# Optimization experiments

Hardware: AMD Instinct MI355X
Metric: run time of the kernel (lower is better)

The kernel has to match this reference:

```python
import jax, jax.numpy as jnp
import numpy as np

EPS_INTERP = 1e-8
EPS_BN = 1e-5


def _bn_relu(x, gamma, beta):
    # x: [B, C, N]; training-mode BatchNorm1d over (B, N) with biased variance
    mean = jnp.mean(x, axis=(0, 2), keepdims=True)
    var = jnp.mean((x - mean) ** 2, axis=(0, 2), keepdims=True)
    xn = (x - mean) / jnp.sqrt(var + EPS_BN)
    return jax.nn.relu(xn * gamma[None, :, None] + beta[None, :, None])


def setup_inputs() -> dict:
    key = jax.random.key(0)
    ks = jax.random.split(key, 8)
    B, N, S, D = 16, 4096, 1024, 128
    return {
        "xyz1": jax.random.normal(ks[0], (B, 3, N), jnp.float32),
        "xyz2": jax.random.normal(ks[1], (B, 3, S), jnp.float32),
        "points1": jax.random.normal(ks[2], (B, D, N), jnp.float32),
        "points2": jax.random.normal(ks[3], (B, D, S), jnp.float32),
        "w0": jax.random.normal(ks[4], (256, 512), jnp.float32) * 0.04,
        "b0": jax.random.normal(ks[5], (256,), jnp.float32) * 0.01,
        "gamma0": jnp.ones((256,), jnp.float32),
        "beta0": jnp.zeros((256,), jnp.float32),
        "w1": jax.random.normal(ks[6], (128, 256), jnp.float32) * 0.06,
        "b1": jax.random.normal(ks[7], (128,), jnp.float32) * 0.01,
        "gamma1": jnp.ones((128,), jnp.float32),
        "beta1": jnp.zeros((128,), jnp.float32),
    }


def reference(xyz1, xyz2, points1, points2, w0, b0, gamma0, beta0, w1, b1, gamma1, beta1):
    # to [B, N, C] layouts
    x1 = jnp.transpose(xyz1, (0, 2, 1))   # [B, N, 3]
    x2 = jnp.transpose(xyz2, (0, 2, 1))   # [B, S, 3]
    p2 = jnp.transpose(points2, (0, 2, 1))  # [B, S, D]
    B, N, _ = x1.shape

    # squared pairwise distances [B, N, S]
    dists = (jnp.sum(x1 ** 2, -1)[:, :, None]
             + jnp.sum(x2 ** 2, -1)[:, None, :]
             - 2.0 * jnp.einsum('bnc,bsc->bns', x1, x2))

    # 3 nearest neighbors (ascending distance)
    neg_d, idx = jax.lax.top_k(-dists, 3)   # idx: [B, N, 3]
    d3 = -neg_d
    recip = 1.0 / (d3 + EPS_INTERP)
    weight = recip / jnp.sum(recip, axis=2, keepdims=True)  # [B, N, 3]

    # gather neighbor features: [B, N, 3, D]
    gathered = jax.vmap(lambda p, i: p[i])(p2, idx)
    # NOTE: this repo flattens the 3 weighted neighbors (no sum) -> [B, N, 3*D]
    interp = (gathered * weight[..., None]).reshape(B, N, -1)

    new_pts = jnp.concatenate([jnp.transpose(points1, (0, 2, 1)), interp], axis=-1)  # [B, N, 512]
    x = jnp.transpose(new_pts, (0, 2, 1))  # [B, 512, N]

    x = _bn_relu(jnp.einsum('oc,bcn->bon', w0, x) + b0[None, :, None], gamma0, beta0)
    x = _bn_relu(jnp.einsum('oc,bcn->bon', w1, x) + b1[None, :, None], gamma1, beta1)
    return x
```

## Files before the change

kernel.cpp:

```cpp
#include <hip/hip_runtime.h>
#include <stdint.h>

typedef unsigned short ushort_t;
typedef __attribute__((ext_vector_type(8))) __bf16 bf16x8;
typedef __attribute__((ext_vector_type(4))) float f32x4;

__device__ __forceinline__ float b2f(ushort_t u) {
    unsigned v = ((unsigned)u) << 16;
    float f;
    __builtin_memcpy(&f, &v, 4);
    return f;
}

__device__ __forceinline__ ushort_t f2b(float f) {
    __bf16 h = (__bf16)f;
    return __builtin_bit_cast(ushort_t, h);
}

__device__ __forceinline__ void gl_lds16(const void* g, void* l) {
    __builtin_amdgcn_global_load_lds((const __attribute__((address_space(1))) void*)g,
                                     (__attribute__((address_space(3))) void*)l, 16, 0, 0);
}

__global__ __launch_bounds__(256) void k_pre(const float* __restrict__ w0, ushort_t* __restrict__ w0b,
                                             const float* __restrict__ w1, ushort_t* __restrict__ w1b,
                                             const float* __restrict__ xyz2, float4* __restrict__ sdat,
                                             const float* __restrict__ points2, ushort_t* __restrict__ p2t) {
    int bid = blockIdx.x;
    int t = threadIdx.x;
    if (bid < 512) {
        int i = bid * 256 + t;
        w0b[i] = f2b(w0[i]);
    } else if (bid < 640) {
        int i = (bid - 512) * 256 + t;
        w1b[i] = f2b(w1[i]);
    } else if (bid < 704) {
        int bb = bid - 640;
        int b = bb & 15, by = bb >> 4;
        int s = by * 256 + t;
        const float* x2 = xyz2 + (size_t)b * 3 * 1024;
        float x = x2[s], y = x2[1024 + s], z = x2[2048 + s];
        float4 v;
        v.x = x; v.y = y; v.z = z;
        v.w = __fadd_rn(__fadd_rn(__fmul_rn(x, x), __fmul_rn(y, y)), __fmul_rn(z, z));
        sdat[(size_t)b * 1024 + s] = v;
    } else {
        int bb = bid - 704;
        int b = bb & 15, sy = bb >> 4;
        int s = sy * 64 + (t & 63);
        int g = t >> 6;
        const float* src = points2 + (size_t)b * 128 * 1024 + s;
        ushort_t* dst = p2t + ((size_t)b * 1024 + s) * 128;
#pragma unroll
        for (int i = 0; i < 4; ++i) {
            int cp = i * 4 + g;
            ushort_t tmp[8];
#pragma unroll
            for (int k = 0; k < 8; ++k) tmp[k] = f2b(src[(size_t)(cp * 8 + k) * 1024]);
            *(uint4*)(dst + cp * 8) = *(const uint4*)tmp;
        }
    }
}

__global__ __launch_bounds__(256) void k_interp(const float* __restrict__ xyz1,
                                                const float4* __restrict__ sdat,
                                                const float* __restrict__ points1,
                                                const ushort_t* __restrict__ p2t,
                                                ushort_t* __restrict__ X) {
    int b = blockIdx.x;
    int n0 = blockIdx.y * 32;
    int t = threadIdx.x;
    int tq = t & 31;
    int slice = t >> 5;
    int wave = t >> 6, lane = t & 63;

    __shared__ __align__(16) char sbuf[16384];
    float4* sP = (float4*)sbuf;
    int*   sidx = (int*)sbuf;
    float* sw   = (float*)(sbuf + 384);
    __shared__ float sD[256 * 3];
    __shared__ int   sI[256 * 3];

    {
        const float4* src = sdat + (size_t)b * 1024;
#pragma unroll
        for (int c = 0; c < 4; ++c) {
            int p = wave * 256 + c * 64 + lane;
            gl_lds16(src + p, sbuf + p * 16);
        }
    }

    int n = n0 + tq;
    float x = xyz1[((size_t)b * 3 + 0) * 4096 + n];
    float y = xyz1[((size_t)b * 3 + 1) * 4096 + n];
    float z = xyz1[((size_t)b * 3 + 2) * 4096 + n];
    float s1 = __fadd_rn(__fadd_rn(__fmul_rn(x, x), __fmul_rn(y, y)), __fmul_rn(z, z));

    __syncthreads();

    const float* p1base = points1 + (size_t)b * 128 * 4096 + n0 + tq;
    float p1v[16];
#pragma unroll
    for (int i = 0; i < 2; ++i)
#pragma unroll
        for (int k = 0; k < 8; ++k)
            p1v[i * 8 + k] = p1base[(size_t)(((i * 8 + slice) * 8) + k) * 4096];

    float d0 = 1e30f, d1 = 1e30f, d2 = 1e30f;
    int i0 = 0, i1 = 0, i2 = 0;
    int sbeg = slice * 128;
    const float4* sdL = sP + sbeg;
#pragma unroll 8
    for (int s = 0; s < 128; ++s) {
        float4 v = sdL[s];
        float dot = fmaf(z, v.z, fmaf(y, v.y, __fmul_rn(x, v.x)));
        float d = __fadd_rn(fmaf(-2.0f, dot, s1), v.w);
        int si = sbeg + s;
        bool c0 = d < d0, c1 = d < d1, c2 = d < d2;
        i2 = c1 ? i1 : (c2 ? si : i2);
        i1 = c0 ? i0 : (c1 ? si : i1);
        i0 = c0 ? si : i0;
        d2 = fminf(fmaxf(d, d1), d2);
        d1 = fminf(fmaxf(d, d0), d1);
        d0 = fminf(d, d0);
    }
    sD[t * 3 + 0] = d0; sD[t * 3 + 1] = d1; sD[t * 3 + 2] = d2;
    sI[t * 3 + 0] = i0; sI[t * 3 + 1] = i1; sI[t * 3 + 2] = i2;

    {
        ushort_t* dstbase = X + (size_t)(b * 4096 + n0 + tq) * 512;
#pragma unroll
        for (int i = 0; i < 2; ++i) {
            int piece = i * 8 + slice;
            ushort_t tmp[8];
#pragma unroll
            for (int k = 0; k < 8; ++k) tmp[k] = f2b(p1v[i * 8 + k]);
            *(uint4*)(dstbase + piece * 8) = *(const uint4*)tmp;
        }
    }
    __syncthreads();

    if (t < 32) {
        int sel0 = -1, sel1 = -1;
        float seld[3]; int seli[3];
#pragma unroll
        for (int r = 0; r < 3; ++r) {
            float bd = 1e38f; int bi = 1 << 30;
            for (int k = 0; k < 24; ++k) {
                int s3 = (k * 0xAAAB) >> 17;
                int rank = k - s3 * 3;
                int base = (s3 * 32 + t) * 3 + rank;
                float cd = sD[base];
                int ci = sI[base];
                bool excl = (ci == sel0) | (ci == sel1);
                bool better = (!excl) & ((cd < bd) | ((cd == bd) & (ci < bi)));
                if (better) { bd = cd; bi = ci; }
            }
            seld[r] = bd; seli[r] = bi;
            if (r == 0) sel0 = bi; else if (r == 1) sel1 = bi;
        }
        float r0 = 1.0f / (seld[0] + 1e-8f);
        float r1 = 1.0f / (seld[1] + 1e-8f);
        float r2 = 1.0f / (seld[2] + 1e-8f);
        float rs = r0 + r1 + r2;
        sw[t * 3 + 0] = r0 / rs; sw[t * 3 + 1] = r1 / rs; sw[t * 3 + 2] = r2 / rs;
        sidx[t * 3 + 0] = seli[0]; sidx[t * 3 + 1] = seli[1]; sidx[t * 3 + 2] = seli[2];
    }
    __syncthreads();

#pragma unroll
    for (int i = 0; i < 6; ++i) {
        int idx = i * 256 + t;
        int q = idx / 48;
        int rem = idx - q * 48;
        int r = rem >> 4;
        int piece = rem & 15;
        int si = sidx[q * 3 + r];
        float wt = sw[q * 3 + r];
        const ushort_t* src = p2t + ((size_t)b * 1024 + si) * 128 + piece * 8;
        uint4 raw = *(const uint4*)src;
        ushort_t* e = (ushort_t*)&raw;
        ushort_t outv[8];
#pragma unroll
        for (int k = 0; k < 8; ++k) outv[k] = f2b(wt * b2f(e[k]));
        ushort_t* dst = X + (size_t)(b * 4096 + n0 + q) * 512 + 128 + r * 128 + piece * 8;
        *(uint4*)dst = *(const uint4*)outv;
    }
}

__global__ __launch_bounds__(256) void k_gemm(const ushort_t* __restrict__ A,
                                              const ushort_t* __restrict__ Bt,
                                              const float* __restrict__ bias,
                                              ushort_t* __restrict__ Y,
                                              float* __restrict__ part_s,
                                              float* __restrict__ part_q,
                                              int Mtot, int K) {
    __shared__ __align__(16) char smem[35840];
    ushort_t* As = (ushort_t*)smem;
    ushort_t* Bs = (ushort_t*)(smem + 16384);
    ushort_t* sY = (ushort_t*)smem;
    float* red_s = (float*)(smem + 34816);
    float* red_q = red_s + 128;

    int t = threadIdx.x;
    int m0 = blockIdx.x * 128;
    int j0 = blockIdx.y * 128;
    int wave = t >> 6, lane = t & 63;
    int wm = wave >> 1, wn = wave & 1;
    int l16 = lane & 15, quad = lane >> 4;

    if (t < 128) { red_s[t] = 0.f; red_q[t] = 0.f; }

    f32x4 acc[4][4] = {};

    int nk = K >> 6;
    for (int kt = 0; kt < nk; ++kt) {
#pragma unroll
        for (int c = 0; c < 4; ++c) {
            int idx = c * 256 + t;
            int row = idx >> 3, kc = idx & 7;
            gl_lds16(A + (size_t)(m0 + row) * K + kt * 64 + kc * 8, As + idx * 8);
            gl_lds16(Bt + (size_t)(j0 + row) * K + kt * 64 + kc * 8, Bs + idx * 8);
        }
        __syncthreads();

#pragma unroll
        for (int kk = 0; kk < 2; ++kk) {
            bf16x8 af[4], bfr[4];
#pragma unroll
            for (int mi = 0; mi < 4; ++mi)
                af[mi] = *(const bf16x8*)(As + (wm * 64 + mi * 16 + l16) * 64 + kk * 32 + quad * 8);
#pragma unroll
            for (int ni = 0; ni < 4; ++ni)
                bfr[ni] = *(const bf16x8*)(Bs + (wn * 64 + ni * 16 + l16) * 64 + kk * 32 + quad * 8);
#pragma unroll
            for (int mi = 0; mi < 4; ++mi)
#pragma unroll
                for (int ni = 0; ni < 4; ++ni)
                    acc[mi][ni] = __builtin_amdgcn_mfma_f32_16x16x32_bf16(af[mi], bfr[ni], acc[mi][ni], 0, 0, 0);
        }
        __syncthreads();
    }

#pragma unroll
    for (int mi = 0; mi < 4; ++mi) {
        int obase = wm * 64 + mi * 16 + quad * 4;
        float bv[4];
#pragma unroll
        for (int r = 0; r < 4; ++r) bv[r] = bias[m0 + obase + r];
        float sr[4] = {0.f, 0.f, 0.f, 0.f}, qr[4] = {0.f, 0.f, 0.f, 0.f};
#pragma unroll
        for (int ni = 0; ni < 4; ++ni) {
            int j_local = wn * 64 + ni * 16 + l16;
            ushort4 pk;
            float v0 = acc[mi][ni][0] + bv[0];
            float v1 = acc[mi][ni][1] + bv[1];
            float v2 = acc[mi][ni][2] + bv[2];
            float v3 = acc[mi][ni][3] + bv[3];
            pk.x = f2b(v0); pk.y = f2b(v1); pk.z = f2b(v2); pk.w = f2b(v3);
            sr[0] += v0; qr[0] += v0 * v0;
            sr[1] += v1; qr[1] += v1 * v1;
            sr[2] += v2; qr[2] += v2 * v2;
            sr[3] += v3; qr[3] += v3 * v3;
            *(ushort4*)(sY + j_local * 136 + obase) = pk;
        }
#pragma unroll
        for (int r = 0; r < 4; ++r) {
            float s = sr[r], q = qr[r];
            s += __shfl_xor(s, 1); s += __shfl_xor(s, 2);
            s += __shfl_xor(s, 4); s += __shfl_xor(s, 8);
            q += __shfl_xor(q, 1); q += __shfl_xor(q, 2);
            q += __shfl_xor(q, 4); q += __shfl_xor(q, 8);
            if (l16 == 0) {
                atomicAdd(&red_s[obase + r], s);
                atomicAdd(&red_q[obase + r], q);
            }
        }
    }
    __syncthreads();

#pragma unroll
    for (int rep = 0; rep < 8; ++rep) {
        int idx = rep * 256 + t;
        int jl = idx >> 4;
        int o8 = idx & 15;
        uint4 vv = *(const uint4*)(sY + jl * 136 + o8 * 8);
        *(uint4*)(Y + (size_t)(j0 + jl) * Mtot + m0 + o8 * 8) = vv;
    }
    if (t < 128) {
        part_s[(size_t)blockIdx.y * Mtot + m0 + t] = red_s[t];
        part_q[(size_t)blockIdx.y * Mtot + m0 + t] = red_q[t];
    }
}

__global__ __launch_bounds__(256) void k_gemmf(const ushort_t* __restrict__ A,
                                               const ushort_t* __restrict__ Y0,
                                               const float* __restrict__ bias,
                                               const float* __restrict__ act_a,
                                               const float* __restrict__ act_b,
                                               ushort_t* __restrict__ Y,
                                               float* __restrict__ part_s,
                                               float* __restrict__ part_q,
                                               int Mtot, int K) {
    __shared__ __align__(16) char smem[35840];
    ushort_t* As = (ushort_t*)smem;
    ushort_t* Bs = (ushort_t*)(smem + 16384);
    float* sa = (float*)(smem + 32768);
    float* sb = (float*)(smem + 33792);
    ushort_t* sY = (ushort_t*)smem;
    float* red_s = (float*)(smem + 34816);
    float* red_q = red_s + 128;

    int t = threadIdx.x;
    int m0 = blockIdx.x * 128;
    int j0 = blockIdx.y * 128;
    int wave = t >> 6, lane = t & 63;
    int wm = wave >> 1, wn = wave & 1;
    int l16 = lane & 15, quad = lane >> 4;

    sa[t] = act_a[t]; sb[t] = act_b[t];
    if (t < 128) { red_s[t] = 0.f; red_q[t] = 0.f; }
    __syncthreads();

    f32x4 acc[4][4] = {};

    int nk = K >> 6;
    for (int kt = 0; kt < nk; ++kt) {
#pragma unroll
        for (int c = 0; c < 4; ++c) {
            int idx = c * 256 + t;
            int row = idx >> 3, kc = idx & 7;
            gl_lds16(A + (size_t)(m0 + row) * K + kt * 64 + kc * 8, As + idx * 8);
        }
#pragma unroll
        for (int c = 0; c < 4; ++c) {
            int idx = c * 256 + t;
            int row = idx >> 3, kc = idx & 7;
            int cbase = kt * 64 + kc * 8;
            uint4 raw = *(const uint4*)(Y0 + (size_t)(j0 + row) * K + cbase);
            ushort_t* e = (ushort_t*)&raw;
            ushort_t outv[8];
#pragma unroll
            for (int k = 0; k < 8; ++k) {
                float v = fmaxf(sa[cbase + k] * b2f(e[k]) + sb[cbase + k], 0.f);
                outv[k] = f2b(v);
            }
            *(uint4*)(Bs + idx * 8) = *(const uint4*)outv;
        }
        __syncthreads();

#pragma unroll
        for (int kk = 0; kk < 2; ++kk) {
            bf16x8 af[4], bfr[4];
#pragma unroll
            for (int mi = 0; mi < 4; ++mi)
                af[mi] = *(const bf16x8*)(As + (wm * 64 + mi * 16 + l16) * 64 + kk * 32 + quad * 8);
#pragma unroll
            for (int ni = 0; ni < 4; ++ni)
                bfr[ni] = *(const bf16x8*)(Bs + (wn * 64 + ni * 16 + l16) * 64 + kk * 32 + quad * 8);
#pragma unroll
            for (int mi = 0; mi < 4; ++mi)
#pragma unroll
                for (int ni = 0; ni < 4; ++ni)
                    acc[mi][ni] = __builtin_amdgcn_mfma_f32_16x16x32_bf16(af[mi], bfr[ni], acc[mi][ni], 0, 0, 0);
        }
        __syncthreads();
    }

#pragma unroll
    for (int mi = 0; mi < 4; ++mi) {
        int obase = wm * 64 + mi * 16 + quad * 4;
        float bv[4];
#pragma unroll
        for (int r = 0; r < 4; ++r) bv[r] = bias[m0 + obase + r];
        float sr[4] = {0.f, 0.f, 0.f, 0.f}, qr[4] = {0.f, 0.f, 0.f, 0.f};
#pragma unroll
        for (int ni = 0; ni < 4; ++ni) {
            int j_local = wn * 64 + ni * 16 + l16;
            ushort4 pk;
            float v0 = acc[mi][ni][0] + bv[0];
            float v1 = acc[mi][ni][1] + bv[1];
            float v2 = acc[mi][ni][2] + bv[2];
            float v3 = acc[mi][ni][3] + bv[3];
            pk.x = f2b(v0); pk.y = f2b(v1); pk.z = f2b(v2); pk.w = f2b(v3);
            sr[0] += v0; qr[0] += v0 * v0;
            sr[1] += v1; qr[1] += v1 * v1;
            sr[2] += v2; qr[2] += v2 * v2;
            sr[3] += v3; qr[3] += v3 * v3;
            *(ushort4*)(sY + j_local * 136 + obase) = pk;
        }
#pragma unroll
        for (int r = 0; r < 4; ++r) {
            float s = sr[r], q = qr[r];
            s += __shfl_xor(s, 1); s += __shfl_xor(s, 2);
            s += __shfl_xor(s, 4); s += __shfl_xor(s, 8);
            q += __shfl_xor(q, 1); q += __shfl_xor(q, 2);
            q += __shfl_xor(q, 4); q += __shfl_xor(q, 8);
            if (l16 == 0) {
                atomicAdd(&red_s[obase + r], s);
                atomicAdd(&red_q[obase + r], q);
            }
        }
    }
    __syncthreads();

#pragma unroll
    for (int rep = 0; rep < 8; ++rep) {
        int idx = rep * 256 + t;
        int jl = idx >> 4;
        int o8 = idx & 15;
        uint4 vv = *(const uint4*)(sY + jl * 136 + o8 * 8);
        *(uint4*)(Y + (size_t)(j0 + jl) * Mtot + m0 + o8 * 8) = vv;
    }
    if (t < 128) {
        part_s[(size_t)blockIdx.y * Mtot + m0 + t] = red_s[t];
        part_q[(size_t)blockIdx.y * Mtot + m0 + t] = red_q[t];
    }
}

__global__ __launch_bounds__(256) void k_bnfin(const float* __restrict__ part_s,
                                               const float* __restrict__ part_q,
                                               int nby,
                                               const float* __restrict__ gamma,
                                               const float* __restrict__ beta,
                                               float* __restrict__ a, float* __restrict__ bb,
                                               int C, float inv_count) {
    __shared__ float rs[4], rq[4];
    int i = blockIdx.x;
    int t = threadIdx.x;
    float s = 0.f, q = 0.f;
    for (int by = t; by < nby; by += 256) {
        s += part_s[(size_t)by * C + i];
        q += part_q[(size_t)by * C + i];
    }
    s += __shfl_xor(s, 1);  q += __shfl_xor(q, 1);
    s += __shfl_xor(s, 2);  q += __shfl_xor(q, 2);
    s += __shfl_xor(s, 4);  q += __shfl_xor(q, 4);
    s += __shfl_xor(s, 8);  q += __shfl_xor(q, 8);
    s += __shfl_xor(s, 16); q += __shfl_xor(q, 16);
    s += __shfl_xor(s, 32); q += __shfl_xor(q, 32);
    int wv = t >> 6, ln = t & 63;
    if (ln == 0) { rs[wv] = s; rq[wv] = q; }
    __syncthreads();
    if (t == 0) {
        s = (rs[0] + rs[1]) + (rs[2] + rs[3]);
        q = (rq[0] + rq[1]) + (rq[2] + rq[3]);
        float mean = s * inv_count;
        float var = q * inv_count - mean * mean;
        float sc = gamma[i] / sqrtf(var + 1e-5f);
        a[i] = sc;
        bb[i] = beta[i] - mean * sc;
    }
}

__global__ __launch_bounds__(256) void k_out(const ushort_t* __restrict__ Y1,
                                             const float* __restrict__ a,
                                             const float* __restrict__ bb,
                                             float* __restrict__ out) {
    __shared__ float sa[128], sb[128];
    int t = threadIdx.x;
    if (t < 128) { sa[t] = a[t]; sb[t] = bb[t]; }
    __syncthreads();
    int b = blockIdx.x;
    int nl = t & 127;
    int half = t >> 7;
    int n = blockIdx.y * 128 + nl;
    const uint4* src = (const uint4*)(Y1 + (size_t)(b * 4096 + n) * 128);
    float* dst = out + (size_t)b * 128 * 4096 + n;
    uint4 raw[8];
#pragma unroll
    for (int p = 0; p < 8; ++p) raw[p] = src[half * 8 + p];
    const ushort_t* e = (const ushort_t*)raw;
#pragma unroll
    for (int c = 0; c < 64; ++c) {
        int ch = half * 64 + c;
        float v = b2f(e[c]);
        v = fmaxf(sa[ch] * v + sb[ch], 0.f);
        dst[(size_t)ch * 4096] = v;
    }
}

extern "C" void kernel_launch(void* const* d_in, const int* in_sizes, int n_in,
                              void* d_out, int out_size, void* d_ws, size_t ws_size,
                              hipStream_t stream) {
    const float* xyz1    = (const float*)d_in[0];
    const float* xyz2    = (const float*)d_in[1];
    const float* points1 = (const float*)d_in[2];
    const float* points2 = (const float*)d_in[3];
    const float* w0      = (const float*)d_in[4];
    const float* b0      = (const float*)d_in[5];
    const float* gamma0  = (const float*)d_in[6];
    const float* beta0   = (const float*)d_in[7];
    const float* w1      = (const float*)d_in[8];
    const float* b1      = (const float*)d_in[9];
    const float* gamma1  = (const float*)d_in[10];
    const float* beta1   = (const float*)d_in[11];
    float* out = (float*)d_out;

    char* ws = (char*)d_ws;
    const size_t OFF_X    = 0;
    const size_t OFF_Y0   = 67108864;
    const size_t OFF_Y1   = 100663296;
    const size_t OFF_P2T  = 117440512;
    const size_t OFF_W0B  = 121634816;
    const size_t OFF_W1B  = 121896960;
    const size_t OFF_AB   = 121962496;
    const size_t OFF_SDAT = 121965568;
    const size_t OFF_PS0  = 122227712;
    const size_t OFF_PQ0  = 122752000;
    const size_t OFF_PS1  = 123276288;
    const size_t OFF_PQ1  = 123538432;

    ushort_t* X    = (ushort_t*)(ws + OFF_X);
    ushort_t* Y0   = (ushort_t*)(ws + OFF_Y0);
    ushort_t* Y1   = (ushort_t*)(ws + OFF_Y1);
    ushort_t* p2t  = (ushort_t*)(ws + OFF_P2T);
    ushort_t* w0b  = (ushort_t*)(ws + OFF_W0B);
    ushort_t* w1b  = (ushort_t*)(ws + OFF_W1B);
    float* ab      = (float*)(ws + OFF_AB);
    float4* sdat   = (float4*)(ws + OFF_SDAT);
    float* ps0 = (float*)(ws + OFF_PS0);
    float* pq0 = (float*)(ws + OFF_PQ0);
    float* ps1 = (float*)(ws + OFF_PS1);
    float* pq1 = (float*)(ws + OFF_PQ1);
    float* a0 = ab;       float* bb0 = ab + 256;
    float* a1 = ab + 512; float* bb1 = ab + 640;

    k_pre<<<960, 256, 0, stream>>>(w0, w0b, w1, w1b, xyz2, sdat, points2, p2t);
    k_interp<<<dim3(16, 128), 256, 0, stream>>>(xyz1, sdat, points1, p2t, X);
    k_gemm<<<dim3(2, 512), 256, 0, stream>>>(w0b, X, b0, Y0, ps0, pq0, 256, 512);
    k_bnfin<<<256, 256, 0, stream>>>(ps0, pq0, 512, gamma0, beta0, a0, bb0, 256, 1.0f / 65536.0f);
    k_gemmf<<<dim3(1, 512), 256, 0, stream>>>(w1b, Y0, b1, a0, bb0, Y1, ps1, pq1, 128, 256);
    k_bnfin<<<128, 256, 0, stream>>>(ps1, pq1, 512, gamma1, beta1, a1, bb1, 128, 1.0f / 65536.0f);
    k_out<<<dim3(16, 32), 256, 0, stream>>>(Y1, a1, bb1, out);
}
```

Baseline: 218.6 us.

## Double points per interp thread and widen first GEMM block to full output dim

k_interp now handles 64 query points per block, with each thread scanning its slice of 128 reference points for two queries, so the LDS-staged xyz2 data is loaded once per 64 points instead of per 32. The first GEMM uses 512-thread blocks covering all 256 output channels per 128-column tile. Each B (activation) tile is therefore read once instead of twice, and the epilogue is written in two halves through shared memory. The trade-off is higher register and LDS pressure, fewer blocks (1024 interp, 512 gemm) and extra barriers in the GEMM epilogue.

```diff
diff --git a/kernel.cpp b/kernel.cpp
--- a/kernel.cpp
+++ b/kernel.cpp
@@ -62,13 +62,13 @@
     }
 }
 
-__global__ __launch_bounds__(256) void k_interp(const float* __restrict__ xyz1,
-                                                const float4* __restrict__ sdat,
-                                                const float* __restrict__ points1,
-                                                const ushort_t* __restrict__ p2t,
-                                                ushort_t* __restrict__ X) {
+__global__ __launch_bounds__(256, 4) void k_interp(const float* __restrict__ xyz1,
+                                                   const float4* __restrict__ sdat,
+                                                   const float* __restrict__ points1,
+                                                   const ushort_t* __restrict__ p2t,
+                                                   ushort_t* __restrict__ X) {
     int b = blockIdx.x;
-    int n0 = blockIdx.y * 32;
+    int n0 = blockIdx.y * 64;
     int t = threadIdx.x;
     int tq = t & 31;
     int slice = t >> 5;
@@ -77,9 +77,9 @@
     __shared__ __align__(16) char sbuf[16384];
     float4* sP = (float4*)sbuf;
     int*   sidx = (int*)sbuf;
-    float* sw   = (float*)(sbuf + 384);
-    __shared__ float sD[256 * 3];
-    __shared__ int   sI[256 * 3];
+    float* sw   = (float*)(sbuf + 768);
+    __shared__ float sD[1536];
+    __shared__ int   sI[1536];
 
     {
         const float4* src = sdat + (size_t)b * 1024;
@@ -90,57 +90,90 @@
         }
     }
 
-    int n = n0 + tq;
-    float x = xyz1[((size_t)b * 3 + 0) * 4096 + n];
-    float y = xyz1[((size_t)b * 3 + 1) * 4096 + n];
-    float z = xyz1[((size_t)b * 3 + 2) * 4096 + n];
-    float s1 = __fadd_rn(__fadd_rn(__fmul_rn(x, x), __fmul_rn(y, y)), __fmul_rn(z, z));
+    int nA = n0 + tq;
+    float xA = xyz1[((size_t)b * 3 + 0) * 4096 + nA];
+    float yA = xyz1[((size_t)b * 3 + 1) * 4096 + nA];
+    float zA = xyz1[((size_t)b * 3 + 2) * 4096 + nA];
+    float s1A = __fadd_rn(__fadd_rn(__fmul_rn(xA, xA), __fmul_rn(yA, yA)), __fmul_rn(zA, zA));
+    float xB = xyz1[((size_t)b * 3 + 0) * 4096 + nA + 32];
+    float yB = xyz1[((size_t)b * 3 + 1) * 4096 + nA + 32];
+    float zB = xyz1[((size_t)b * 3 + 2) * 4096 + nA + 32];
+    float s1B = __fadd_rn(__fadd_rn(__fmul_rn(xB, xB), __fmul_rn(yB, yB)), __fmul_rn(zB, zB));
 
     __syncthreads();
 
     const float* p1base = points1 + (size_t)b * 128 * 4096 + n0 + tq;
-    float p1v[16];
+    float p1v[32];
 #pragma unroll
     for (int i = 0; i < 2; ++i)
 #pragma unroll
-        for (int k = 0; k < 8; ++k)
-            p1v[i * 8 + k] = p1base[(size_t)(((i * 8 + slice) * 8) + k) * 4096];
-
-    float d0 = 1e30f, d1 = 1e30f, d2 = 1e30f;
-    int i0 = 0, i1 = 0, i2 = 0;
+        for (int k = 0; k < 8; ++k) {
+            size_t off = (size_t)(((i * 8 + slice) * 8) + k) * 4096;
+            p1v[i * 8 + k]      = p1base[off];
+            p1v[16 + i * 8 + k] = p1base[off + 32];
+        }
+
+    float d0A = 1e30f, d1A = 1e30f, d2A = 1e30f;
+    int i0A = 0, i1A = 0, i2A = 0;
+    float d0B = 1e30f, d1B = 1e30f, d2B = 1e30f;
+    int i0B = 0, i1B = 0, i2B = 0;
     int sbeg = slice * 128;
     const float4* sdL = sP + sbeg;
-#pragma unroll 8
+#pragma unroll 4
     for (int s = 0; s < 128; ++s) {
         float4 v = sdL[s];
-        float dot = fmaf(z, v.z, fmaf(y, v.y, __fmul_rn(x, v.x)));
-        float d = __fadd_rn(fmaf(-2.0f, dot, s1), v.w);
         int si = sbeg + s;
-        bool c0 = d < d0, c1 = d < d1, c2 = d < d2;
-        i2 = c1 ? i1 : (c2 ? si : i2);
-        i1 = c0 ? i0 : (c1 ? si : i1);
-        i0 = c0 ? si : i0;
-        d2 = fminf(fmaxf(d, d1), d2);
-        d1 = fminf(fmaxf(d, d0), d1);
-        d0 = fminf(d, d0);
-    }
-    sD[t * 3 + 0] = d0; sD[t * 3 + 1] = d1; sD[t * 3 + 2] = d2;
-    sI[t * 3 + 0] = i0; sI[t * 3 + 1] = i1; sI[t * 3 + 2] = i2;
-
+        {
+            float dot = fmaf(zA, v.z, fmaf(yA, v.y, __fmul_rn(xA, v.x)));
+            float d = __fadd_rn(fmaf(-2.0f, dot, s1A), v.w);
+            bool c0 = d < d0A, c1 = d < d1A, c2 = d < d2A;
+            i2A = c1 ? i1A : (c2 ? si : i2A);
+            i1A = c0 ? i0A : (c1 ? si : i1A);
+            i0A = c0 ? si : i0A;
+            d2A = fminf(fmaxf(d, d1A), d2A);
+            d1A = fminf(fmaxf(d, d0A), d1A);
+            d0A = fminf(d, d0A);
+        }
+        {
+            float dot = fmaf(zB, v.z, fmaf(yB, v.y, __fmul_rn(xB, v.x)));
+            float d = __fadd_rn(fmaf(-2.0f, dot, s1B), v.w);
+            bool c0 = d < d0B, c1 = d < d1B, c2 = d < d2B;
+            i2B = c1 ? i1B : (c2 ? si : i2B);
+            i1B = c0 ? i0B : (c1 ? si : i1B);
+            i0B = c0 ? si : i0B;
+            d2B = fminf(fmaxf(d, d1B), d2B);
+            d1B = fminf(fmaxf(d, d0B), d1B);
+            d0B = fminf(d, d0B);
+        }
+    }
     {
-        ushort_t* dstbase = X + (size_t)(b * 4096 + n0 + tq) * 512;
+        int baseA = (slice * 64 + tq) * 3;
+        int baseB = (slice * 64 + tq + 32) * 3;
+        sD[baseA + 0] = d0A; sD[baseA + 1] = d1A; sD[baseA + 2] = d2A;
+        sI[baseA + 0] = i0A; sI[baseA + 1] = i1A; sI[baseA + 2] = i2A;
+        sD[baseB + 0] = d0B; sD[baseB + 1] = d1B; sD[baseB + 2] = d2B;
+        sI[baseB + 0] = i0B; sI[baseB + 1] = i1B; sI[baseB + 2] = i2B;
+    }
+
+    {
+        ushort_t* dstA = X + (size_t)(b * 4096 + n0 + tq) * 512;
+        ushort_t* dstB = X + (size_t)(b * 4096 + n0 + tq + 32) * 512;
 #pragma unroll
         for (int i = 0; i < 2; ++i) {
             int piece = i * 8 + slice;
-            ushort_t tmp[8];
-#pragma unroll
-            for (int k = 0; k < 8; ++k) tmp[k] = f2b(p1v[i * 8 + k]);
-            *(uint4*)(dstbase + piece * 8) = *(const uint4*)tmp;
-        }
-    }
-    __syncthreads();
-
-    if (t < 32) {
+            ushort_t tA[8], tB[8];
+#pragma unroll
+            for (int k = 0; k < 8; ++k) {
+                tA[k] = f2b(p1v[i * 8 + k]);
+                tB[k] = f2b(p1v[16 + i * 8 + k]);
+            }
+            *(uint4*)(dstA + piece * 8) = *(const uint4*)tA;
+            *(uint4*)(dstB + piece * 8) = *(const uint4*)tB;
+        }
+    }
+    __syncthreads();
+
+    if (t < 64) {
         int sel0 = -1, sel1 = -1;
         float seld[3]; int seli[3];
 #pragma unroll
@@ -149,7 +182,7 @@
             for (int k = 0; k < 24; ++k) {
                 int s3 = (k * 0xAAAB) >> 17;
                 int rank = k - s3 * 3;
-                int base = (s3 * 32 + t) * 3 + rank;
+                int base = (s3 * 64 + t) * 3 + rank;
                 float cd = sD[base];
                 int ci = sI[base];
                 bool excl = (ci == sel0) | (ci == sel1);
@@ -169,7 +202,7 @@
     __syncthreads();
 
 #pragma unroll
-    for (int i = 0; i < 6; ++i) {
+    for (int i = 0; i < 12; ++i) {
         int idx = i * 256 + t;
         int q = idx / 48;
         int rem = idx - q * 48;
@@ -188,28 +221,27 @@
     }
 }
 
-__global__ __launch_bounds__(256) void k_gemm(const ushort_t* __restrict__ A,
-                                              const ushort_t* __restrict__ Bt,
-                                              const float* __restrict__ bias,
-                                              ushort_t* __restrict__ Y,
-                                              float* __restrict__ part_s,
-                                              float* __restrict__ part_q,
-                                              int Mtot, int K) {
-    __shared__ __align__(16) char smem[35840];
+__global__ __launch_bounds__(512, 4) void k_gemm(const ushort_t* __restrict__ A,
+                                                 const ushort_t* __restrict__ Bt,
+                                                 const float* __restrict__ bias,
+                                                 ushort_t* __restrict__ Y,
+                                                 float* __restrict__ part_s,
+                                                 float* __restrict__ part_q,
+                                                 int Mtot, int K) {
+    __shared__ __align__(16) char smem[51200];
     ushort_t* As = (ushort_t*)smem;
-    ushort_t* Bs = (ushort_t*)(smem + 16384);
+    ushort_t* Bs = (ushort_t*)(smem + 32768);
     ushort_t* sY = (ushort_t*)smem;
-    float* red_s = (float*)(smem + 34816);
-    float* red_q = red_s + 128;
+    float* red_s = (float*)(smem + 49152);
+    float* red_q = red_s + 256;
 
     int t = threadIdx.x;
-    int m0 = blockIdx.x * 128;
-    int j0 = blockIdx.y * 128;
+    int j0 = blockIdx.x * 128;
     int wave = t >> 6, lane = t & 63;
     int wm = wave >> 1, wn = wave & 1;
     int l16 = lane & 15, quad = lane >> 4;
 
-    if (t < 128) { red_s[t] = 0.f; red_q[t] = 0.f; }
+    if (t < 256) { red_s[t] = 0.f; red_q[t] = 0.f; }
 
     f32x4 acc[4][4] = {};
 
@@ -217,9 +249,14 @@
     for (int kt = 0; kt < nk; ++kt) {
 #pragma unroll
         for (int c = 0; c < 4; ++c) {
-            int idx = c * 256 + t;
+            int idx = c * 512 + t;
             int row = idx >> 3, kc = idx & 7;
-            gl_lds16(A + (size_t)(m0 + row) * K + kt * 64 + kc * 8, As + idx * 8);
+            gl_lds16(A + (size_t)row * K + kt * 64 + kc * 8, As + idx * 8);
+        }
+#pragma unroll
+        for (int c = 0; c < 2; ++c) {
+            int idx = c * 512 + t;
+            int row = idx >> 3, kc = idx & 7;
             gl_lds16(Bt + (size_t)(j0 + row) * K + kt * 64 + kc * 8, Bs + idx * 8);
         }
         __syncthreads();
@@ -243,53 +280,59 @@
     }
 
 #pragma unroll
-    for (int mi = 0; mi < 4; ++mi) {
-        int obase = wm * 64 + mi * 16 + quad * 4;
-        float bv[4];
-#pragma unroll
-        for (int r = 0; r < 4; ++r) bv[r] = bias[m0 + obase + r];
-        float sr[4] = {0.f, 0.f, 0.f, 0.f}, qr[4] = {0.f, 0.f, 0.f, 0.f};
-#pragma unroll
-        for (int ni = 0; ni < 4; ++ni) {
-            int j_local = wn * 64 + ni * 16 + l16;
-            ushort4 pk;
-            float v0 = acc[mi][ni][0] + bv[0];
-            float v1 = acc[mi][ni][1] + bv[1];
-            float v2 = acc[mi][ni][2] + bv[2];
-            float v3 = acc[mi][ni][3] + bv[3];
-            pk.x = f2b(v0); pk.y = f2b(v1); pk.z = f2b(v2); pk.w = f2b(v3);
-            sr[0] += v0; qr[0] += v0 * v0;
-            sr[1] += v1; qr[1] += v1 * v1;
-            sr[2] += v2; qr[2] += v2 * v2;
-            sr[3] += v3; qr[3] += v3 * v3;
-            *(ushort4*)(sY + j_local * 136 + obase) = pk;
-        }
-#pragma unroll
-        for (int r = 0; r < 4; ++r) {
-            float s = sr[r], q = qr[r];
-            s += __shfl_xor(s, 1); s += __shfl_xor(s, 2);
-            s += __shfl_xor(s, 4); s += __shfl_xor(s, 8);
-            q += __shfl_xor(q, 1); q += __shfl_xor(q, 2);
-            q += __shfl_xor(q, 4); q += __shfl_xor(q, 8);
-            if (l16 == 0) {
-                atomicAdd(&red_s[obase + r], s);
-                atomicAdd(&red_q[obase + r], q);
+    for (int h = 0; h < 2; ++h) {
+        if ((wm >> 1) == h) {
+#pragma unroll
+            for (int mi = 0; mi < 4; ++mi) {
+                int obase = wm * 64 + mi * 16 + quad * 4;
+                int ocol = obase - h * 128;
+                float bv[4];
+#pragma unroll
+                for (int r = 0; r < 4; ++r) bv[r] = bias[obase + r];
+                float sr[4] = {0.f, 0.f, 0.f, 0.f}, qr[4] = {0.f, 0.f, 0.f, 0.f};
+#pragma unroll
+                for (int ni = 0; ni < 4; ++ni) {
+                    int j_local = wn * 64 + ni * 16 + l16;
+                    ushort4 pk;
+                    float v0 = acc[mi][ni][0] + bv[0];
+                    float v1 = acc[mi][ni][1] + bv[1];
+                    float v2 = acc[mi][ni][2] + bv[2];
+                    float v3 = acc[mi][ni][3] + bv[3];
+                    pk.x = f2b(v0); pk.y = f2b(v1); pk.z = f2b(v2); pk.w = f2b(v3);
+                    sr[0] += v0; qr[0] += v0 * v0;
+                    sr[1] += v1; qr[1] += v1 * v1;
+                    sr[2] += v2; qr[2] += v2 * v2;
+                    sr[3] += v3; qr[3] += v3 * v3;
+                    *(ushort4*)(sY + j_local * 136 + ocol) = pk;
+                }
+#pragma unroll
+                for (int r = 0; r < 4; ++r) {
+                    float s = sr[r], q = qr[r];
+                    s += __shfl_xor(s, 1); s += __shfl_xor(s, 2);
+                    s += __shfl_xor(s, 4); s += __shfl_xor(s, 8);
+                    q += __shfl_xor(q, 1); q += __shfl_xor(q, 2);
+                    q += __shfl_xor(q, 4); q += __shfl_xor(q, 8);
+                    if (l16 == 0) {
+                        atomicAdd(&red_s[obase + r], s);
+                        atomicAdd(&red_q[obase + r], q);
+                    }
+                }
             }
         }
-    }
-    __syncthreads();
-
-#pragma unroll
-    for (int rep = 0; rep < 8; ++rep) {
-        int idx = rep * 256 + t;
-        int jl = idx >> 4;
-        int o8 = idx & 15;
-        uint4 vv = *(const uint4*)(sY + jl * 136 + o8 * 8);
-        *(uint4*)(Y + (size_t)(j0 + jl) * Mtot + m0 + o8 * 8) = vv;
-    }
-    if (t < 128) {
-        part_s[(size_t)blockIdx.y * Mtot + m0 + t] = red_s[t];
-        part_q[(size_t)blockIdx.y * Mtot + m0 + t] = red_q[t];
+        __syncthreads();
+#pragma unroll
+        for (int rep = 0; rep < 4; ++rep) {
+            int idx = rep * 512 + t;
+            int jl = idx >> 4;
+            int o8 = idx & 15;
+            uint4 vv = *(const uint4*)(sY + jl * 136 + o8 * 8);
+            *(uint4*)(Y + (size_t)(j0 + jl) * Mtot + h * 128 + o8 * 8) = vv;
+        }
+        __syncthreads();
+    }
+    if (t < 256) {
+        part_s[(size_t)blockIdx.x * Mtot + t] = red_s[t];
+        part_q[(size_t)blockIdx.x * Mtot + t] = red_q[t];
     }
 }
 
@@ -527,8 +570,8 @@
     float* a1 = ab + 512; float* bb1 = ab + 640;
 
     k_pre<<<960, 256, 0, stream>>>(w0, w0b, w1, w1b, xyz2, sdat, points2, p2t);
-    k_interp<<<dim3(16, 128), 256, 0, stream>>>(xyz1, sdat, points1, p2t, X);
-    k_gemm<<<dim3(2, 512), 256, 0, stream>>>(w0b, X, b0, Y0, ps0, pq0, 256, 512);
+    k_interp<<<dim3(16, 64), 256, 0, stream>>>(xyz1, sdat, points1, p2t, X);
+    k_gemm<<<512, 512, 0, stream>>>(w0b, X, b0, Y0, ps0, pq0, 256, 512);
     k_bnfin<<<256, 256, 0, stream>>>(ps0, pq0, 512, gamma0, beta0, a0, bb0, 256, 1.0f / 65536.0f);
     k_gemmf<<<dim3(1, 512), 256, 0, stream>>>(w1b, Y0, b1, a0, bb0, Y1, ps1, pq1, 128, 256);
     k_bnfin<<<128, 256, 0, stream>>>(ps1, pq1, 512, gamma1, beta1, a1, bb1, 128, 1.0f / 65536.0f);
```

After: 212.7 us. 1.03x faster.

## Fuse neighbor gather into first GEMM and fold BN finalize via atomics

Applied to the files above, without the earlier changes.

The interpolation kernel no longer writes the 512-wide concatenated X matrix. It stores only the points1 slice plus the neighbor indices and weights, and the first GEMM gathers and weights the p2t rows while loading its B tiles. The first GEMM now uses 512-thread blocks covering all 256 output channels, and BN statistics are accumulated into global sums with atomics. This removes both k_bnfin launches, because the scale and shift are computed inside k_gemmf and k_out. The aim is to cut the large X write and read traffic and the launch overhead, at the cost of gather loads inside the GEMM loop that go through registers and are not overlapped, plus float atomics that make the sums order-nondeterministic.

```diff
diff --git a/kernel.cpp b/kernel.cpp
--- a/kernel.cpp
+++ b/kernel.cpp
@@ -25,7 +25,8 @@
 __global__ __launch_bounds__(256) void k_pre(const float* __restrict__ w0, ushort_t* __restrict__ w0b,
                                              const float* __restrict__ w1, ushort_t* __restrict__ w1b,
                                              const float* __restrict__ xyz2, float4* __restrict__ sdat,
-                                             const float* __restrict__ points2, ushort_t* __restrict__ p2t) {
+                                             const float* __restrict__ points2, ushort_t* __restrict__ p2t,
+                                             float* __restrict__ zb) {
     int bid = blockIdx.x;
     int t = threadIdx.x;
     if (bid < 512) {
@@ -44,7 +45,7 @@
         v.x = x; v.y = y; v.z = z;
         v.w = __fadd_rn(__fadd_rn(__fmul_rn(x, x), __fmul_rn(y, y)), __fmul_rn(z, z));
         sdat[(size_t)b * 1024 + s] = v;
-    } else {
+    } else if (bid < 960) {
         int bb = bid - 704;
         int b = bb & 15, sy = bb >> 4;
         int s = sy * 64 + (t & 63);
@@ -59,14 +60,18 @@
             for (int k = 0; k < 8; ++k) tmp[k] = f2b(src[(size_t)(cp * 8 + k) * 1024]);
             *(uint4*)(dst + cp * 8) = *(const uint4*)tmp;
         }
+    } else {
+        zb[t] = 0.f; zb[256 + t] = 0.f;
+        if (t < 128) { zb[512 + t] = 0.f; zb[640 + t] = 0.f; }
     }
 }
 
 __global__ __launch_bounds__(256) void k_interp(const float* __restrict__ xyz1,
                                                 const float4* __restrict__ sdat,
                                                 const float* __restrict__ points1,
-                                                const ushort_t* __restrict__ p2t,
-                                                ushort_t* __restrict__ X) {
+                                                ushort_t* __restrict__ Xp1,
+                                                int* __restrict__ sidxg,
+                                                float* __restrict__ swg) {
     int b = blockIdx.x;
     int n0 = blockIdx.y * 32;
     int t = threadIdx.x;
@@ -76,10 +81,8 @@
 
     __shared__ __align__(16) char sbuf[16384];
     float4* sP = (float4*)sbuf;
-    int*   sidx = (int*)sbuf;
-    float* sw   = (float*)(sbuf + 384);
-    __shared__ float sD[256 * 3];
-    __shared__ int   sI[256 * 3];
+    __shared__ float sD[768];
+    __shared__ int   sI[768];
 
     {
         const float4* src = sdat + (size_t)b * 1024;
@@ -128,7 +131,7 @@
     sI[t * 3 + 0] = i0; sI[t * 3 + 1] = i1; sI[t * 3 + 2] = i2;
 
     {
-        ushort_t* dstbase = X + (size_t)(b * 4096 + n0 + tq) * 512;
+        ushort_t* dstbase = Xp1 + (size_t)(b * 4096 + n0 + tq) * 128;
 #pragma unroll
         for (int i = 0; i < 2; ++i) {
             int piece = i * 8 + slice;
@@ -163,41 +166,168 @@
         float r1 = 1.0f / (seld[1] + 1e-8f);
         float r2 = 1.0f / (seld[2] + 1e-8f);
         float rs = r0 + r1 + r2;
-        sw[t * 3 + 0] = r0 / rs; sw[t * 3 + 1] = r1 / rs; sw[t * 3 + 2] = r2 / rs;
-        sidx[t * 3 + 0] = seli[0]; sidx[t * 3 + 1] = seli[1]; sidx[t * 3 + 2] = seli[2];
-    }
-    __syncthreads();
-
-#pragma unroll
-    for (int i = 0; i < 6; ++i) {
-        int idx = i * 256 + t;
-        int q = idx / 48;
-        int rem = idx - q * 48;
-        int r = rem >> 4;
-        int piece = rem & 15;
-        int si = sidx[q * 3 + r];
-        float wt = sw[q * 3 + r];
-        const ushort_t* src = p2t + ((size_t)b * 1024 + si) * 128 + piece * 8;
-        uint4 raw = *(const uint4*)src;
-        ushort_t* e = (ushort_t*)&raw;
-        ushort_t outv[8];
-#pragma unroll
-        for (int k = 0; k < 8; ++k) outv[k] = f2b(wt * b2f(e[k]));
-        ushort_t* dst = X + (size_t)(b * 4096 + n0 + q) * 512 + 128 + r * 128 + piece * 8;
-        *(uint4*)dst = *(const uint4*)outv;
-    }
-}
-
-__global__ __launch_bounds__(256) void k_gemm(const ushort_t* __restrict__ A,
-                                              const ushort_t* __restrict__ Bt,
-                                              const float* __restrict__ bias,
-                                              ushort_t* __restrict__ Y,
-                                              float* __restrict__ part_s,
-                                              float* __restrict__ part_q,
-                                              int Mtot, int K) {
+        size_t base = (size_t)(b * 4096 + n0 + t) * 3;
+        sidxg[base + 0] = seli[0]; sidxg[base + 1] = seli[1]; sidxg[base + 2] = seli[2];
+        swg[base + 0] = r0 / rs; swg[base + 1] = r1 / rs; swg[base + 2] = r2 / rs;
+    }
+}
+
+__global__ __launch_bounds__(512, 4) void k_gemm(const ushort_t* __restrict__ A,
+                                                 const ushort_t* __restrict__ Xp1,
+                                                 const ushort_t* __restrict__ p2t,
+                                                 const int* __restrict__ sidxg,
+                                                 const float* __restrict__ swg,
+                                                 const float* __restrict__ bias,
+                                                 ushort_t* __restrict__ Y,
+                                                 float* __restrict__ gs,
+                                                 float* __restrict__ gq,
+                                                 int Mtot, int K) {
+    __shared__ __align__(16) char smem[54784];
+    ushort_t* As = (ushort_t*)smem;
+    ushort_t* Bs = (ushort_t*)(smem + 32768);
+    ushort_t* sY = (ushort_t*)smem;
+    float* red_s = (float*)(smem + 49152);
+    float* red_q = red_s + 256;
+    int*   lsi   = (int*)(smem + 51200);
+    float* lsw   = (float*)(smem + 52736);
+
+    int t = threadIdx.x;
+    int j0 = blockIdx.x * 128;
+    int b = j0 >> 12;
+    int wave = t >> 6, lane = t & 63;
+    int wm = wave >> 1, wn = wave & 1;
+    int l16 = lane & 15, quad = lane >> 4;
+
+    if (t < 256) { red_s[t] = 0.f; red_q[t] = 0.f; }
+    if (t < 384) { lsi[t] = sidxg[(size_t)j0 * 3 + t]; lsw[t] = swg[(size_t)j0 * 3 + t]; }
+
+    f32x4 acc[4][4] = {};
+
+    int nk = K >> 6;
+    for (int kt = 0; kt < nk; ++kt) {
+#pragma unroll
+        for (int c = 0; c < 4; ++c) {
+            int idx = c * 512 + t;
+            int row = idx >> 3, kc = idx & 7;
+            gl_lds16(A + (size_t)row * K + kt * 64 + kc * 8, As + idx * 8);
+        }
+        if (kt < 2) {
+#pragma unroll
+            for (int c = 0; c < 2; ++c) {
+                int idx = c * 512 + t;
+                int row = idx >> 3, kc = idx & 7;
+                gl_lds16(Xp1 + (size_t)(j0 + row) * 128 + kt * 64 + kc * 8, Bs + idx * 8);
+            }
+        } else {
+            int r = (kt - 2) >> 1, h = (kt - 2) & 1;
+#pragma unroll
+            for (int c = 0; c < 2; ++c) {
+                int idx = c * 512 + t;
+                int row = idx >> 3, kc = idx & 7;
+                int si = lsi[row * 3 + r];
+                float w = lsw[row * 3 + r];
+                const ushort_t* src = p2t + ((size_t)b * 1024 + si) * 128 + h * 64 + kc * 8;
+                uint4 raw = *(const uint4*)src;
+                ushort_t* e = (ushort_t*)&raw;
+                ushort_t outv[8];
+#pragma unroll
+                for (int k = 0; k < 8; ++k) outv[k] = f2b(w * b2f(e[k]));
+                *(uint4*)(Bs + idx * 8) = *(const uint4*)outv;
+            }
+        }
+        __syncthreads();
+
+#pragma unroll
+        for (int kk = 0; kk < 2; ++kk) {
+            bf16x8 af[4], bfr[4];
+#pragma unroll
+            for (int mi = 0; mi < 4; ++mi)
+                af[mi] = *(const bf16x8*)(As + (wm * 64 + mi * 16 + l16) * 64 + kk * 32 + quad * 8);
+#pragma unroll
+            for (int ni = 0; ni < 4; ++ni)
+                bfr[ni] = *(const bf16x8*)(Bs + (wn * 64 + ni * 16 + l16) * 64 + kk * 32 + quad * 8);
+#pragma unroll
+            for (int mi = 0; mi < 4; ++mi)
+#pragma unroll
+                for (int ni = 0; ni < 4; ++ni)
+                    acc[mi][ni] = __builtin_amdgcn_mfma_f32_16x16x32_bf16(af[mi], bfr[ni], acc[mi][ni], 0, 0, 0);
+        }
+        __syncthreads();
+    }
+
+#pragma unroll
+    for (int h = 0; h < 2; ++h) {
+        if ((wm >> 1) == h) {
+#pragma unroll
+            for (int mi = 0; mi < 4; ++mi) {
+                int obase = wm * 64 + mi * 16 + quad * 4;
+                int ocol = obase - h * 128;
+                float bv[4];
+#pragma unroll
+                for (int r = 0; r < 4; ++r) bv[r] = bias[obase + r];
+                float sr[4] = {0.f, 0.f, 0.f, 0.f}, qr[4] = {0.f, 0.f, 0.f, 0.f};
+#pragma unroll
+                for (int ni = 0; ni < 4; ++ni) {
+                    int j_local = wn * 64 + ni * 16 + l16;
+                    ushort4 pk;
+                    float v0 = acc[mi][ni][0] + bv[0];
+                    float v1 = acc[mi][ni][1] + bv[1];
+                    float v2 = acc[mi][ni][2] + bv[2];
+                    float v3 = acc[mi][ni][3] + bv[3];
+                    pk.x = f2b(v0); pk.y = f2b(v1); pk.z = f2b(v2); pk.w = f2b(v3);
+                    sr[0] += v0; qr[0] += v0 * v0;
+                    sr[1] += v1; qr[1] += v1 * v1;
+                    sr[2] += v2; qr[2] += v2 * v2;
+                    sr[3] += v3; qr[3] += v3 * v3;
+                    *(ushort4*)(sY + j_local * 136 + ocol) = pk;
+                }
+#pragma unroll
+                for (int r = 0; r < 4; ++r) {
+                    float s = sr[r], q = qr[r];
+                    s += __shfl_xor(s, 1); s += __shfl_xor(s, 2);
+                    s += __shfl_xor(s, 4); s += __shfl_xor(s, 8);
+                    q += __shfl_xor(q, 1); q += __shfl_xor(q, 2);
+                    q += __shfl_xor(q, 4); q += __shfl_xor(q, 8);
+                    if (l16 == 0) {
+                        atomicAdd(&red_s[obase + r], s);
+                        atomicAdd(&red_q[obase + r], q);
+                    }
+                }
+            }
+        }
+        __syncthreads();
+#pragma unroll
+        for (int rep = 0; rep < 4; ++rep) {
+            int idx = rep * 512 + t;
+            int jl = idx >> 4;
+            int o8 = idx & 15;
+            uint4 vv = *(const uint4*)(sY + jl * 136 + o8 * 8);
+            *(uint4*)(Y + (size_t)(j0 + jl) * Mtot + h * 128 + o8 * 8) = vv;
+        }
+        __syncthreads();
+    }
+    if (t < 256) {
+        atomicAdd(&gs[t], red_s[t]);
+        atomicAdd(&gq[t], red_q[t]);
+    }
+}
+
+__global__ __launch_bounds__(256) void k_gemmf(const ushort_t* __restrict__ A,
+                                               const ushort_t* __restrict__ Y0,
+                                               const float* __restrict__ bias,
+                                               const float* __restrict__ gamma0,
+                                               const float* __restrict__ beta0,
+                                               const float* __restrict__ gs0,
+                                               const float* __restrict__ gq0,
+                                               ushort_t* __restrict__ Y,
+                                               float* __restrict__ gs1,
+                                               float* __restrict__ gq1,
+                                               int Mtot, int K) {
     __shared__ __align__(16) char smem[35840];
     ushort_t* As = (ushort_t*)smem;
     ushort_t* Bs = (ushort_t*)(smem + 16384);
+    float* sa = (float*)(smem + 32768);
+    float* sb = (float*)(smem + 33792);
     ushort_t* sY = (ushort_t*)smem;
     float* red_s = (float*)(smem + 34816);
     float* red_q = red_s + 128;
@@ -209,7 +339,16 @@
     int wm = wave >> 1, wn = wave & 1;
     int l16 = lane & 15, quad = lane >> 4;
 
+    {
+        float s = gs0[t], q = gq0[t];
+        float mean = s * (1.0f / 65536.0f);
+        float var = q * (1.0f / 65536.0f) - mean * mean;
+        float sc = gamma0[t] / sqrtf(var + 1e-5f);
+        sa[t] = sc;
+        sb[t] = beta0[t] - mean * sc;
+    }
     if (t < 128) { red_s[t] = 0.f; red_q[t] = 0.f; }
+    __syncthreads();
 
     f32x4 acc[4][4] = {};
 
@@ -220,7 +359,21 @@
             int idx = c * 256 + t;
             int row = idx >> 3, kc = idx & 7;
             gl_lds16(A + (size_t)(m0 + row) * K + kt * 64 + kc * 8, As + idx * 8);
-            gl_lds16(Bt + (size_t)(j0 + row) * K + kt * 64 + kc * 8, Bs + idx * 8);
+        }
+#pragma unroll
+        for (int c = 0; c < 4; ++c) {
+            int idx = c * 256 + t;
+            int row = idx >> 3, kc = idx & 7;
+            int cbase = kt * 64 + kc * 8;
+            uint4 raw = *(const uint4*)(Y0 + (size_t)(j0 + row) * K + cbase);
+            ushort_t* e = (ushort_t*)&raw;
+            ushort_t outv[8];
+#pragma unroll
+            for (int k = 0; k < 8; ++k) {
+                float v = fmaxf(sa[cbase + k] * b2f(e[k]) + sb[cbase + k], 0.f);
+                outv[k] = f2b(v);
+            }
+            *(uint4*)(Bs + idx * 8) = *(const uint4*)outv;
         }
         __syncthreads();
 
@@ -288,178 +441,27 @@
         *(uint4*)(Y + (size_t)(j0 + jl) * Mtot + m0 + o8 * 8) = vv;
     }
     if (t < 128) {
-        part_s[(size_t)blockIdx.y * Mtot + m0 + t] = red_s[t];
-        part_q[(size_t)blockIdx.y * Mtot + m0 + t] = red_q[t];
-    }
-}
-
-__global__ __launch_bounds__(256) void k_gemmf(const ushort_t* __restrict__ A,
-                                               const ushort_t* __restrict__ Y0,
-                                               const float* __restrict__ bias,
-                                               const float* __restrict__ act_a,
-                                               const float* __restrict__ act_b,
-                                               ushort_t* __restrict__ Y,
-                                               float* __restrict__ part_s,
-                                               float* __restrict__ part_q,
-                                               int Mtot, int K) {
-    __shared__ __align__(16) char smem[35840];
-    ushort_t* As = (ushort_t*)smem;
-    ushort_t* Bs = (ushort_t*)(smem + 16384);
-    float* sa = (float*)(smem + 32768);
-    float* sb = (float*)(smem + 33792);
-    ushort_t* sY = (ushort_t*)smem;
-    float* red_s = (float*)(smem + 34816);
-    float* red_q = red_s + 128;
-
-    int t = threadIdx.x;
-    int m0 = blockIdx.x * 128;
-    int j0 = blockIdx.y * 128;
-    int wave = t >> 6, lane = t & 63;
-    int wm = wave >> 1, wn = wave & 1;
-    int l16 = lane & 15, quad = lane >> 4;
-
-    sa[t] = act_a[t]; sb[t] = act_b[t];
-    if (t < 128) { red_s[t] = 0.f; red_q[t] = 0.f; }
-    __syncthreads();
-
-    f32x4 acc[4][4] = {};
-
-    int nk = K >> 6;
-    for (int kt = 0; kt < nk; ++kt) {
-#pragma unroll
-        for (int c = 0; c < 4; ++c) {
-            int idx = c * 256 + t;
-            int row = idx >> 3, kc = idx & 7;
-            gl_lds16(A + (size_t)(m0 + row) * K + kt * 64 + kc * 8, As + idx * 8);
-        }
-#pragma unroll
-        for (int c = 0; c < 4; ++c) {
-            int idx = c * 256 + t;
-            int row = idx >> 3, kc = idx & 7;
-            int cbase = kt * 64 + kc * 8;
-            uint4 raw = *(const uint4*)(Y0 + (size_t)(j0 + row) * K + cbase);
-            ushort_t* e = (ushort_t*)&raw;
-            ushort_t outv[8];
-#pragma unroll
-            for (int k = 0; k < 8; ++k) {
-                float v = fmaxf(sa[cbase + k] * b2f(e[k]) + sb[cbase + k], 0.f);
-                outv[k] = f2b(v);
-            }
-            *(uint4*)(Bs + idx * 8) = *(const uint4*)outv;
-        }
-        __syncthreads();
-
-#pragma unroll
-        for (int kk = 0; kk < 2; ++kk) {
-            bf16x8 af[4], bfr[4];
-#pragma unroll
-            for (int mi = 0; mi < 4; ++mi)
-                af[mi] = *(const bf16x8*)(As + (wm * 64 + mi * 16 + l16) * 64 + kk * 32 + quad * 8);
-#pragma unroll
-            for (int ni = 0; ni < 4; ++ni)
-                bfr[ni] = *(const bf16x8*)(Bs + (wn * 64 + ni * 16 + l16) * 64 + kk * 32 + quad * 8);
-#pragma unroll
-            for (int mi = 0; mi < 4; ++mi)
-#pragma unroll
-                for (int ni = 0; ni < 4; ++ni)
-                    acc[mi][ni] = __builtin_amdgcn_mfma_f32_16x16x32_bf16(af[mi], bfr[ni], acc[mi][ni], 0, 0, 0);
-        }
-        __syncthreads();
-    }
-
-#pragma unroll
-    for (int mi = 0; mi < 4; ++mi) {
-        int obase = wm * 64 + mi * 16 + quad * 4;
-        float bv[4];
-#pragma unroll
-        for (int r = 0; r < 4; ++r) bv[r] = bias[m0 + obase + r];
-        float sr[4] = {0.f, 0.f, 0.f, 0.f}, qr[4] = {0.f, 0.f, 0.f, 0.f};
-#pragma unroll
-        for (int ni = 0; ni < 4; ++ni) {
-            int j_local = wn * 64 + ni * 16 + l16;
-            ushort4 pk;
-            float v0 = acc[mi][ni][0] + bv[0];
-            float v1 = acc[mi][ni][1] + bv[1];
-            float v2 = acc[mi][ni][2] + bv[2];
-            float v3 = acc[mi][ni][3] + bv[3];
-            pk.x = f2b(v0); pk.y = f2b(v1); pk.z = f2b(v2); pk.w = f2b(v3);
-            sr[0] += v0; qr[0] += v0 * v0;
-            sr[1] += v1; qr[1] += v1 * v1;
-            sr[2] += v2; qr[2] += v2 * v2;
-            sr[3] += v3; qr[3] += v3 * v3;
-            *(ushort4*)(sY + j_local * 136 + obase) = pk;
-        }
-#pragma unroll
-        for (int r = 0; r < 4; ++r) {
-            float s = sr[r], q = qr[r];
-            s += __shfl_xor(s, 1); s += __shfl_xor(s, 2);
-            s += __shfl_xor(s, 4); s += __shfl_xor(s, 8);
-            q += __shfl_xor(q, 1); q += __shfl_xor(q, 2);
-            q += __shfl_xor(q, 4); q += __shfl_xor(q, 8);
-            if (l16 == 0) {
-                atomicAdd(&red_s[obase + r], s);
-                atomicAdd(&red_q[obase + r], q);
-            }
-        }
-    }
-    __syncthreads();
-
-#pragma unroll
-    for (int rep = 0; rep < 8; ++rep) {
-        int idx = rep * 256 + t;
-        int jl = idx >> 4;
-        int o8 = idx & 15;
-        uint4 vv = *(const uint4*)(sY + jl * 136 + o8 * 8);
-        *(uint4*)(Y + (size_t)(j0 + jl) * Mtot + m0 + o8 * 8) = vv;
-    }
-    if (t < 128) {
-        part_s[(size_t)blockIdx.y * Mtot + m0 + t] = red_s[t];
-        part_q[(size_t)blockIdx.y * Mtot + m0 + t] = red_q[t];
-    }
-}
-
-__global__ __launch_bounds__(256) void k_bnfin(const float* __restrict__ part_s,
-                                               const float* __restrict__ part_q,
-                                               int nby,
-                                               const float* __restrict__ gamma,
-                                               const float* __restrict__ beta,
-                                               float* __restrict__ a, float* __restrict__ bb,
-                                               int C, float inv_count) {
-    __shared__ float rs[4], rq[4];
-    int i = blockIdx.x;
-    int t = threadIdx.x;
-    float s = 0.f, q = 0.f;
-    for (int by = t; by < nby; by += 256) {
-        s += part_s[(size_t)by * C + i];
-        q += part_q[(size_t)by * C + i];
-    }
-    s += __shfl_xor(s, 1);  q += __shfl_xor(q, 1);
-    s += __shfl_xor(s, 2);  q += __shfl_xor(q, 2);
-    s += __shfl_xor(s, 4);  q += __shfl_xor(q, 4);
-    s += __shfl_xor(s, 8);  q += __shfl_xor(q, 8);
-    s += __shfl_xor(s, 16); q += __shfl_xor(q, 16);
-    s += __shfl_xor(s, 32); q += __shfl_xor(q, 32);
-    int wv = t >> 6, ln = t & 63;
-    if (ln == 0) { rs[wv] = s; rq[wv] = q; }
-    __syncthreads();
-    if (t == 0) {
-        s = (rs[0] + rs[1]) + (rs[2] + rs[3]);
-        q = (rq[0] + rq[1]) + (rq[2] + rq[3]);
-        float mean = s * inv_count;
-        float var = q * inv_count - mean * mean;
-        float sc = gamma[i] / sqrtf(var + 1e-5f);
-        a[i] = sc;
-        bb[i] = beta[i] - mean * sc;
+        atomicAdd(&gs1[m0 + t], red_s[t]);
+        atomicAdd(&gq1[m0 + t], red_q[t]);
     }
 }
 
 __global__ __launch_bounds__(256) void k_out(const ushort_t* __restrict__ Y1,
-                                             const float* __restrict__ a,
-                                             const float* __restrict__ bb,
+                                             const float* __restrict__ gs1,
+                                             const float* __restrict__ gq1,
+                                             const float* __restrict__ gamma1,
+                                             const float* __restrict__ beta1,
                                              float* __restrict__ out) {
     __shared__ float sa[128], sb[128];
     int t = threadIdx.x;
-    if (t < 128) { sa[t] = a[t]; sb[t] = bb[t]; }
+    if (t < 128) {
+        float s = gs1[t], q = gq1[t];
+        float mean = s * (1.0f / 65536.0f);
+        float var = q * (1.0f / 65536.0f) - mean * mean;
+        float sc = gamma1[t] / sqrtf(var + 1e-5f);
+        sa[t] = sc;
+        sb[t] = beta1[t] - mean * sc;
+    }
     __syncthreads();
     int b = blockIdx.x;
     int nl = t & 127;
@@ -498,7 +500,9 @@
     float* out = (float*)d_out;
 
     char* ws = (char*)d_ws;
-    const size_t OFF_X    = 0;
+    const size_t OFF_XP1  = 0;
+    const size_t OFF_SIDX = 16777216;
+    const size_t OFF_SW   = 17563648;
     const size_t OFF_Y0   = 67108864;
     const size_t OFF_Y1   = 100663296;
     const size_t OFF_P2T  = 117440512;
@@ -506,12 +510,10 @@
     const size_t OFF_W1B  = 121896960;
     const size_t OFF_AB   = 121962496;
     const size_t OFF_SDAT = 121965568;
-    const size_t OFF_PS0  = 122227712;
-    const size_t OFF_PQ0  = 122752000;
-    const size_t OFF_PS1  = 123276288;
-    const size_t OFF_PQ1  = 123538432;
-
-    ushort_t* X    = (ushort_t*)(ws + OFF_X);
+
+    ushort_t* Xp1  = (ushort_t*)(ws + OFF_XP1);
+    int*   sidxg   = (int*)(ws + OFF_SIDX);
+    float* swg     = (float*)(ws + OFF_SW);
     ushort_t* Y0   = (ushort_t*)(ws + OFF_Y0);
     ushort_t* Y1   = (ushort_t*)(ws + OFF_Y1);
     ushort_t* p2t  = (ushort_t*)(ws + OFF_P2T);
@@ -519,18 +521,12 @@
     ushort_t* w1b  = (ushort_t*)(ws + OFF_W1B);
     float* ab      = (float*)(ws + OFF_AB);
     float4* sdat   = (float4*)(ws + OFF_SDAT);
-    float* ps0 = (float*)(ws + OFF_PS0);
-    float* pq0 = (float*)(ws + OFF_PQ0);
-    float* ps1 = (float*)(ws + OFF_PS1);
-    float* pq1 = (float*)(ws + OFF_PQ1);
-    float* a0 = ab;       float* bb0 = ab + 256;
-    float* a1 = ab + 512; float* bb1 = ab + 640;
-
-    k_pre<<<960, 256, 0, stream>>>(w0, w0b, w1, w1b, xyz2, sdat, points2, p2t);
-    k_interp<<<dim3(16, 128), 256, 0, stream>>>(xyz1, sdat, points1, p2t, X);
-    k_gemm<<<dim3(2, 512), 256, 0, stream>>>(w0b, X, b0, Y0, ps0, pq0, 256, 512);
-    k_bnfin<<<256, 256, 0, stream>>>(ps0, pq0, 512, gamma0, beta0, a0, bb0, 256, 1.0f / 65536.0f);
-    k_gemmf<<<dim3(1, 512), 256, 0, stream>>>(w1b, Y0, b1, a0, bb0, Y1, ps1, pq1, 128, 256);
-    k_bnfin<<<128, 256, 0, stream>>>(ps1, pq1, 512, gamma1, beta1, a1, bb1, 128, 1.0f / 65536.0f);
-    k_out<<<dim3(16, 32), 256, 0, stream>>>(Y1, a1, bb1, out);
-}
+    float* gs0 = ab;        float* gq0 = ab + 256;
+    float* gs1 = ab + 512;  float* gq1 = ab + 640;
+
+    k_pre<<<961, 256, 0, stream>>>(w0, w0b, w1, w1b, xyz2, sdat, points2, p2t, ab);
+    k_interp<<<dim3(16, 128), 256, 0, stream>>>(xyz1, sdat, points1, Xp1, sidxg, swg);
+    k_gemm<<<512, 512, 0, stream>>>(w0b, Xp1, p2t, sidxg, swg, b0, Y0, gs0, gq0, 256, 512);
+    k_gemmf<<<dim3(1, 512), 256, 0, stream>>>(w1b, Y0, b1, gamma0, beta0, gs0, gq0, Y1, gs1, gq1, 128, 256);
+    k_out<<<dim3(16, 32), 256, 0, stream>>>(Y1, gs1, gq1, gamma1, beta1, out);
+}
```

Measured after the change: 224.6 us. 1.03x slower.
